# Kernel optimization log

Measured on AMD Instinct MI355X. Metric: run time of the kernel, lower is better.

Reference implementation:

```python
import jax, jax.numpy as jnp
import numpy as np

NUM_HEADS = 8
EPS = 1e-12  # torch F.normalize eps


def _l2norm(t):
    n = jnp.linalg.norm(t, axis=-1, keepdims=True)
    return t / jnp.maximum(n, EPS)


def setup_inputs() -> dict:
    key = jax.random.key(0)
    k1, k2, k3 = jax.random.split(key, 3)
    B, T, N, D = 16, 12, 1024, 128
    x = jax.random.normal(k1, (B, T, N, D), dtype=jnp.float32)
    # Linear(model_dim, 3*model_dim, bias=False): stored as (D, 3D) for x @ W
    W_qkv = jax.random.normal(k2, (D, 3 * D), dtype=jnp.float32) * (1.0 / np.sqrt(D))
    W_out = jax.random.normal(k3, (D, D), dtype=jnp.float32) * (1.0 / np.sqrt(D))
    b_out = jnp.zeros((D,), dtype=jnp.float32)
    return {"x": x, "W_qkv": W_qkv, "W_out": W_out, "b_out": b_out}


def reference(x, W_qkv, W_out, b_out):
    B, T, N, D = x.shape
    H = NUM_HEADS
    hd = D // H
    qkv = x @ W_qkv                                  # (B,T,N,3D)
    q, k, v = jnp.split(qkv, 3, axis=-1)
    # split heads + flatten (B,T) -> b = B*T, matching torch stack/flatten
    qs = _l2norm(q.reshape(B * T, N, H, hd))          # (b,N,H,m)
    ks = _l2norm(k.reshape(B * T, N, H, hd))
    vs = v.reshape(B * T, N, H, hd)
    # linear attention: running kv sum + normalizer
    kvs = jnp.einsum('blhm,blhd->bhmd', ks, vs)       # (b,H,m,d)
    attn_num = jnp.einsum('bnhm,bhmd->bnhd', qs, kvs) + N * vs
    ks_sum = jnp.sum(ks, axis=1)                      # (b,H,m)
    normalizer = jnp.einsum('bnhm,bhm->bnh', qs, ks_sum)[..., None] + N
    out = attn_num / normalizer                       # (b,N,H,d)
    out = out.reshape(B, T, N, D)
    return out @ W_out + b_out
```

## Files before the change

### kernel.cpp

```cpp
#include <hip/hip_runtime.h>
#include <hip/hip_bf16.h>

#define NBATCH 192
#define SEQ    1024
#define DIM    128
#define NH     8
#define EPS    1e-12f

typedef short bf16x8 __attribute__((ext_vector_type(8)));
typedef float f32x4  __attribute__((ext_vector_type(4)));

#define KVSP_F   1572864
#define KSSUM_F  24576
#define WSWT_OFF ((size_t)(KVSP_F + KSSUM_F) * 4)

static __device__ __forceinline__ unsigned short f2bf(float f) {
    unsigned u = __builtin_bit_cast(unsigned, f);
    u += 0x7fff + ((u >> 16) & 1);
    return (unsigned short)(u >> 16);
}

static __device__ __forceinline__ unsigned pk2(float a, float b) {
    __hip_bfloat162 h = __float22bfloat162_rn(make_float2(a, b));
    unsigned r;
    __builtin_memcpy(&r, &h, 4);
    return r;
}
static __device__ __forceinline__ unsigned short bf1(float a) {
    __hip_bfloat16 h = __float2bfloat16(a);
    unsigned short r;
    __builtin_memcpy(&r, &h, 2);
    return r;
}

template <int CTRL>
static __device__ __forceinline__ float dpp_add(float v) {
    int j = __builtin_amdgcn_mov_dpp(__builtin_bit_cast(int, v), CTRL, 0xf, 0xf, false);
    return v + __builtin_bit_cast(float, j);
}
static __device__ __forceinline__ float r16sum(float v) {
    v = dpp_add<0xB1>(v);
    v = dpp_add<0x4E>(v);
    v = dpp_add<0x141>(v);
    v = dpp_add<0x140>(v);
    return v;
}

static __device__ __forceinline__ int strip_addr(int row, int el) {
    return row * 32 + ((((el >> 3) ^ (row & 3)) << 3) | (el & 7));
}

static __device__ __forceinline__ uint2 pack4(float a, float b, float c, float d) {
    uint2 r;
    r.x = pk2(a, b);
    r.y = pk2(c, d);
    return r;
}

static __device__ __forceinline__ bf16x8 cvt8(float4 a, float4 b) {
    uint4 u;
    u.x = pk2(a.x, a.y); u.y = pk2(a.z, a.w);
    u.z = pk2(b.x, b.y); u.w = pk2(b.z, b.w);
    return __builtin_bit_cast(bf16x8, u);
}

static __device__ __forceinline__ bf16x8 gfrag(const unsigned short* __restrict__ wT,
                                               int ct, int ks, int lane) {
    return *reinterpret_cast<const bf16x8*>(wT + ((ct * 4 + ks) * 64 + lane) * 8);
}

__global__ __launch_bounds__(256) void k0_prep(const float* __restrict__ Wqkv,
                                               const float* __restrict__ Wout,
                                               float* __restrict__ kssum_ws,
                                               unsigned short* __restrict__ wsWT) {
    int i = blockIdx.x * 256 + threadIdx.x;
    if (i < KSSUM_F) kssum_ws[i] = 0.0f;
    int which = i >> 14, e = i & 16383;
    int j = e & 7, f = e >> 3;
    int n15 = f & 15, q = (f >> 4) & 3, ks = (f >> 6) & 3, ct = f >> 8;
    int k = ks * 32 + q * 8 + j, n = ct * 16 + n15;
    float v = (which < 3) ? Wqkv[k * 384 + which * 128 + n] : Wout[k * 128 + n];
    wsWT[i] = f2bf(v);
}

__global__ __launch_bounds__(512, 4) void k1_kv(const float* __restrict__ x,
                                                const unsigned short* __restrict__ wsWT,
                                                float* __restrict__ kvs_part,
                                                float* __restrict__ kssum_ws) {
    __shared__ float redf[16384];
    __shared__ unsigned short strips[8192];
    int t = threadIdx.x, w = t >> 6, lane = t & 63, q = lane >> 4, n15 = lane & 15;
    int b = blockIdx.x >> 2, seg = blockIdx.x & 3;
    const unsigned short* wkT = wsWT + 16384;
    const unsigned short* wvT = wsWT + 32768;
    unsigned short* knS = strips + w * 1024;
    unsigned short* vS  = knS + 512;

    bf16x8 ah[2][4];
#pragma unroll
    for (int rs = 0; rs < 2; ++rs) {
        int row = seg * 256 + w * 32 + rs * 16 + n15;
        const float* xr = x + (size_t)(b * SEQ + row) * DIM;
#pragma unroll
        for (int ks = 0; ks < 4; ++ks) {
            float4 p0 = *reinterpret_cast<const float4*>(xr + ks * 32 + q * 8);
            float4 p1 = *reinterpret_cast<const float4*>(xr + ks * 32 + q * 8 + 4);
            ah[rs][ks] = cvt8(p0, p1);
        }
    }

#pragma unroll 1
    for (int ct = 0; ct < 8; ++ct) {
        f32x4 ka[2] = {(f32x4){0,0,0,0}, (f32x4){0,0,0,0}};
        f32x4 va[2] = {(f32x4){0,0,0,0}, (f32x4){0,0,0,0}};
#pragma unroll
        for (int ks = 0; ks < 4; ++ks) {
            bf16x8 kb = gfrag(wkT, ct, ks, lane);
            bf16x8 vb = gfrag(wvT, ct, ks, lane);
#pragma unroll
            for (int rs = 0; rs < 2; ++rs) {
                ka[rs] = __builtin_amdgcn_mfma_f32_16x16x32_bf16(ah[rs][ks], kb, ka[rs], 0, 0, 0);
                va[rs] = __builtin_amdgcn_mfma_f32_16x16x32_bf16(ah[rs][ks], vb, va[rs], 0, 0, 0);
            }
        }
        float ksum = 0.f;
#pragma unroll
        for (int rs = 0; rs < 2; ++rs) {
            float kn[4];
#pragma unroll
            for (int r = 0; r < 4; ++r) {
                float val = ka[rs][r];
                float ssq = r16sum(val * val);
                float di  = 1.0f / fmaxf(sqrtf(ssq), EPS);
                kn[r] = val * di;
                ksum += kn[r];
            }
            *reinterpret_cast<uint2*>(knS + strip_addr(n15, rs * 16 + q * 4)) =
                pack4(kn[0], kn[1], kn[2], kn[3]);
            *reinterpret_cast<uint2*>(vS + strip_addr(n15, rs * 16 + q * 4)) =
                pack4(va[rs][0], va[rs][1], va[rs][2], va[rs][3]);
        }
        bf16x8 aK = *reinterpret_cast<const bf16x8*>(knS + strip_addr(n15, q * 8));
        bf16x8 bV = *reinterpret_cast<const bf16x8*>(vS + strip_addr(n15, q * 8));
        f32x4 kacc = __builtin_amdgcn_mfma_f32_16x16x32_bf16(aK, bV, (f32x4){0,0,0,0}, 0, 0, 0);
#pragma unroll
        for (int r = 0; r < 4; ++r)
            redf[w * 2048 + ct * 256 + (q * 4 + r) * 16 + n15] = kacc[r];
        float s = ksum;
        s += __shfl_xor(s, 16); s += __shfl_xor(s, 32);
        if (lane < 16) atomicAdd(&kssum_ws[b * 128 + ct * 16 + n15], s);
    }

    __syncthreads();
    float* myPart = kvs_part + (size_t)blockIdx.x * 2048;
#pragma unroll
    for (int i = 0; i < 4; ++i) {
        int el = i * 512 + t;
        float s = 0.f;
#pragma unroll
        for (int ww = 0; ww < 8; ++ww) s += redf[ww * 2048 + el];
        myPart[el] = s;
    }
}

__global__ __launch_bounds__(512, 4) void k2_out(const float* __restrict__ x,
                                                 const unsigned short* __restrict__ wsWT,
                                                 const float* __restrict__ kvs_part,
                                                 const float* __restrict__ kssum_ws,
                                                 const float* __restrict__ bout,
                                                 float* __restrict__ out) {
    __shared__ unsigned short lds[24576];
    unsigned short* kvsT   = lds;
    unsigned short* strips = lds + 4096;
    unsigned short* tile   = lds + 8192;
    int t = threadIdx.x, w = t >> 6, lane = t & 63, q = lane >> 4, n15 = lane & 15;
    int b = blockIdx.x >> 2, seg = blockIdx.x & 3, rowbase = seg * 256;
    const unsigned short* wqT = wsWT;
    const unsigned short* wvT = wsWT + 32768;
    const unsigned short* woT = wsWT + 49152;

    {
        int row = t >> 2, part = t & 3, h = row >> 4, d = row & 15;
        const float* kp = kvs_part + (size_t)b * 4 * 2048;
        unsigned es[8];
#pragma unroll
        for (int j = 0; j < 8; j += 2) {
            int m0 = part * 8 + j;
            float lo = 0.f, hi = 0.f;
#pragma unroll
            for (int s = 0; s < 4; ++s) {
                if (m0     < 16) lo += kp[s * 2048 + h * 256 + m0 * 16 + d];
                if (m0 + 1 < 16) hi += kp[s * 2048 + h * 256 + (m0 + 1) * 16 + d];
            }
            es[j] = pk2(lo, hi);
        }
        uint4 v = {es[0], es[2], es[4], es[6]};
        *reinterpret_cast<uint4*>(kvsT + row * 32 + ((part ^ (row & 3)) << 3)) = v;
    }

    unsigned short* myS = strips + w * 512;
    unsigned short* tw  = tile + w * 2048;
    {
        uint2 z = {0, 0};
        *reinterpret_cast<uint2*>(myS + strip_addr(n15, 16 + q * 4)) = z;
    }
    __syncthreads();

    bf16x8 qb[4];
#pragma unroll
    for (int ks = 0; ks < 4; ++ks) qb[ks] = gfrag(wqT, 0, ks, lane);
    float kssh = kssum_ws[b * 128 + n15];

#pragma unroll 1
    for (int rs = 0; rs < 2; ++rs) {
        bf16x8 ahc[4];
        {
            int row = rowbase + w * 32 + rs * 16 + n15;
            const float* xr = x + (size_t)(b * SEQ + row) * DIM;
#pragma unroll
            for (int ks = 0; ks < 4; ++ks) {
                float4 p0 = *reinterpret_cast<const float4*>(xr + ks * 32 + q * 8);
                float4 p1 = *reinterpret_cast<const float4*>(xr + ks * 32 + q * 8 + 4);
                ahc[ks] = cvt8(p0, p1);
            }
        }

#pragma unroll 1
        for (int h = 0; h < 8; ++h) {
            bf16x8 vb0 = gfrag(wvT, h, 0, lane);
            bf16x8 vb1 = gfrag(wvT, h, 1, lane);
            bf16x8 vb2 = gfrag(wvT, h, 2, lane);
            bf16x8 vb3 = gfrag(wvT, h, 3, lane);
            f32x4 qa = (f32x4){0,0,0,0};
            qa = __builtin_amdgcn_mfma_f32_16x16x32_bf16(ahc[0], qb[0], qa, 0, 0, 0);
            qa = __builtin_amdgcn_mfma_f32_16x16x32_bf16(ahc[1], qb[1], qa, 0, 0, 0);
            qa = __builtin_amdgcn_mfma_f32_16x16x32_bf16(ahc[2], qb[2], qa, 0, 0, 0);
            qa = __builtin_amdgcn_mfma_f32_16x16x32_bf16(ahc[3], qb[3], qa, 0, 0, 0);
            f32x4 va = (f32x4){0,0,0,0};
            va = __builtin_amdgcn_mfma_f32_16x16x32_bf16(ahc[0], vb0, va, 0, 0, 0);
            va = __builtin_amdgcn_mfma_f32_16x16x32_bf16(ahc[1], vb1, va, 0, 0, 0);
            va = __builtin_amdgcn_mfma_f32_16x16x32_bf16(ahc[2], vb2, va, 0, 0, 0);
            va = __builtin_amdgcn_mfma_f32_16x16x32_bf16(ahc[3], vb3, va, 0, 0, 0);

            int hn = (h + 1) & 7;
            bf16x8 nqb0 = gfrag(wqT, hn, 0, lane);
            bf16x8 nqb1 = gfrag(wqT, hn, 1, lane);
            bf16x8 nqb2 = gfrag(wqT, hn, 2, lane);
            bf16x8 nqb3 = gfrag(wqT, hn, 3, lane);
            float nkss = kssum_ws[b * 128 + hn * 16 + n15];

            float pv[4];
#pragma unroll
            for (int r = 0; r < 4; ++r) {
                float val = qa[r];
                float ssq = r16sum(val * val);
                float tt  = r16sum(val * kssh);
                float di  = 1.0f / fmaxf(sqrtf(ssq), EPS);
                float inv = 1.0f / (tt * di + (float)SEQ);
                pv[r] = val * di * inv;
                va[r] *= (float)SEQ * inv;
            }
#pragma unroll
            for (int r = 0; r < 4; ++r)
                myS[strip_addr(q * 4 + r, n15)] = bf1(pv[r]);
            bf16x8 aq = *reinterpret_cast<const bf16x8*>(myS + strip_addr(n15, q * 8));
            bf16x8 bk = *reinterpret_cast<const bf16x8*>(kvsT + strip_addr(h * 16 + n15, q * 8));
            va = __builtin_amdgcn_mfma_f32_16x16x32_bf16(aq, bk, va, 0, 0, 0);
#pragma unroll
            for (int r = 0; r < 4; ++r) {
                int rt = q * 4 + r;
                int colg = h * 2 + (n15 >> 3);
                tw[rt * 128 + (((colg ^ rt) << 3) | (n15 & 7))] = bf1(va[r]);
            }
            qb[0] = nqb0; qb[1] = nqb1; qb[2] = nqb2; qb[3] = nqb3;
            kssh = nkss;
        }

        bf16x8 ap[4];
#pragma unroll
        for (int ks = 0; ks < 4; ++ks)
            ap[ks] = *reinterpret_cast<const bf16x8*>(
                tw + n15 * 128 + ((((ks << 2) + q) ^ n15) << 3));
#pragma unroll 1
        for (int ct = 0; ct < 8; ++ct) {
            f32x4 oa = (f32x4){0,0,0,0};
#pragma unroll
            for (int ks = 0; ks < 4; ++ks) {
                bf16x8 bb = gfrag(woT, ct, ks, lane);
                oa = __builtin_amdgcn_mfma_f32_16x16x32_bf16(ap[ks], bb, oa, 0, 0, 0);
            }
            float bo = bout[ct * 16 + n15];
#pragma unroll
            for (int r = 0; r < 4; ++r) {
                int row = rowbase + w * 32 + rs * 16 + q * 4 + r;
                out[(size_t)(b * SEQ + row) * DIM + ct * 16 + n15] = oa[r] + bo;
            }
        }
    }
}

extern "C" void kernel_launch(void* const* d_in, const int* in_sizes, int n_in,
                              void* d_out, int out_size, void* d_ws, size_t ws_size,
                              hipStream_t stream) {
    const float* x    = (const float*)d_in[0];
    const float* Wqkv = (const float*)d_in[1];
    const float* Wout = (const float*)d_in[2];
    const float* bout = (const float*)d_in[3];
    float* out = (float*)d_out;

    float* kvs_part = (float*)d_ws;
    float* kssum_ws = kvs_part + KVSP_F;
    unsigned short* wsWT = (unsigned short*)((char*)d_ws + WSWT_OFF);

    k0_prep<<<dim3(256), dim3(256), 0, stream>>>(Wqkv, Wout, kssum_ws, wsWT);
    k1_kv<<<dim3(768), dim3(512), 0, stream>>>(x, wsWT, kvs_part, kssum_ws);
    k2_out<<<dim3(768), dim3(512), 0, stream>>>(x, wsWT, kvs_part, kssum_ws, bout, out);
}
```

Before: 281.5 us.

## Precompute q·ksum via Wq·ksum projection matrix with one MFMA per row strip

Rather than reducing q·ksum with a 16-lane shuffle reduction for every head, the output kernel precomputes U = Wq_h·ksum_h per batch (a 128x8 matrix) in LDS. It then gets all heads' normalizer dot products with four MFMAs per row strip, picking each head's value by lane shuffle. This removes one r16sum reduction per element and the prefetched-Wq register pipeline, and loads the Q/V weight fragments inline instead. The cost is extra per-block setup reading fp32 Wqkv, more LDS, and an unnormalized-q dot product rounded through bf16, which changes numerics slightly.

Measured after the change: 297.4 us. +5.6%, slower.

```diff
diff --git a/kernel.cpp b/kernel.cpp
--- a/kernel.cpp
+++ b/kernel.cpp
@@ -167,12 +167,14 @@
                                                  const unsigned short* __restrict__ wsWT,
                                                  const float* __restrict__ kvs_part,
                                                  const float* __restrict__ kssum_ws,
+                                                 const float* __restrict__ Wqkv,
                                                  const float* __restrict__ bout,
                                                  float* __restrict__ out) {
-    __shared__ unsigned short lds[24576];
+    __shared__ unsigned short lds[26624];
     unsigned short* kvsT   = lds;
     unsigned short* strips = lds + 4096;
-    unsigned short* tile   = lds + 8192;
+    unsigned short* uLds   = lds + 8192;
+    unsigned short* tile   = lds + 10240;
     int t = threadIdx.x, w = t >> 6, lane = t & 63, q = lane >> 4, n15 = lane & 15;
     int b = blockIdx.x >> 2, seg = blockIdx.x & 3, rowbase = seg * 256;
     const unsigned short* wqT = wsWT;
@@ -198,6 +200,22 @@
         *reinterpret_cast<uint4*>(kvsT + row * 32 + ((part ^ (row & 3)) << 3)) = v;
     }
 
+    {
+#pragma unroll
+        for (int p4 = 0; p4 < 4; ++p4) {
+            int p = t * 4 + p4;
+            int c = p >> 4, h = p & 15;
+            float u = 0.f;
+            if (h < 8) {
+                const float* wr = Wqkv + c * 384 + h * 16;
+                const float* ks = kssum_ws + b * 128 + h * 16;
+#pragma unroll
+                for (int m = 0; m < 16; ++m) u += wr[m] * ks[m];
+            }
+            uLds[(((c >> 5) * 4 + ((c >> 3) & 3)) * 16 + h) * 8 + (c & 7)] = bf1(u);
+        }
+    }
+
     unsigned short* myS = strips + w * 512;
     unsigned short* tw  = tile + w * 2048;
     {
@@ -205,11 +223,6 @@
         *reinterpret_cast<uint2*>(myS + strip_addr(n15, 16 + q * 4)) = z;
     }
     __syncthreads();
-
-    bf16x8 qb[4];
-#pragma unroll
-    for (int ks = 0; ks < 4; ++ks) qb[ks] = gfrag(wqT, 0, ks, lane);
-    float kssh = kssum_ws[b * 128 + n15];
 
 #pragma unroll 1
     for (int rs = 0; rs < 2; ++rs) {
@@ -224,37 +237,31 @@
                 ahc[ks] = cvt8(p0, p1);
             }
         }
+        f32x4 ttC = (f32x4){0,0,0,0};
+#pragma unroll
+        for (int ks = 0; ks < 4; ++ks) {
+            bf16x8 uf = *reinterpret_cast<const bf16x8*>(uLds + (ks * 64 + lane) * 8);
+            ttC = __builtin_amdgcn_mfma_f32_16x16x32_bf16(ahc[ks], uf, ttC, 0, 0, 0);
+        }
 
 #pragma unroll 1
         for (int h = 0; h < 8; ++h) {
-            bf16x8 vb0 = gfrag(wvT, h, 0, lane);
-            bf16x8 vb1 = gfrag(wvT, h, 1, lane);
-            bf16x8 vb2 = gfrag(wvT, h, 2, lane);
-            bf16x8 vb3 = gfrag(wvT, h, 3, lane);
             f32x4 qa = (f32x4){0,0,0,0};
-            qa = __builtin_amdgcn_mfma_f32_16x16x32_bf16(ahc[0], qb[0], qa, 0, 0, 0);
-            qa = __builtin_amdgcn_mfma_f32_16x16x32_bf16(ahc[1], qb[1], qa, 0, 0, 0);
-            qa = __builtin_amdgcn_mfma_f32_16x16x32_bf16(ahc[2], qb[2], qa, 0, 0, 0);
-            qa = __builtin_amdgcn_mfma_f32_16x16x32_bf16(ahc[3], qb[3], qa, 0, 0, 0);
             f32x4 va = (f32x4){0,0,0,0};
-            va = __builtin_amdgcn_mfma_f32_16x16x32_bf16(ahc[0], vb0, va, 0, 0, 0);
-            va = __builtin_amdgcn_mfma_f32_16x16x32_bf16(ahc[1], vb1, va, 0, 0, 0);
-            va = __builtin_amdgcn_mfma_f32_16x16x32_bf16(ahc[2], vb2, va, 0, 0, 0);
-            va = __builtin_amdgcn_mfma_f32_16x16x32_bf16(ahc[3], vb3, va, 0, 0, 0);
-
-            int hn = (h + 1) & 7;
-            bf16x8 nqb0 = gfrag(wqT, hn, 0, lane);
-            bf16x8 nqb1 = gfrag(wqT, hn, 1, lane);
-            bf16x8 nqb2 = gfrag(wqT, hn, 2, lane);
-            bf16x8 nqb3 = gfrag(wqT, hn, 3, lane);
-            float nkss = kssum_ws[b * 128 + hn * 16 + n15];
-
+#pragma unroll
+            for (int ks = 0; ks < 4; ++ks) {
+                bf16x8 qb = gfrag(wqT, h, ks, lane);
+                bf16x8 vb = gfrag(wvT, h, ks, lane);
+                qa = __builtin_amdgcn_mfma_f32_16x16x32_bf16(ahc[ks], qb, qa, 0, 0, 0);
+                va = __builtin_amdgcn_mfma_f32_16x16x32_bf16(ahc[ks], vb, va, 0, 0, 0);
+            }
+            int srcl = (lane & 48) | h;
             float pv[4];
 #pragma unroll
             for (int r = 0; r < 4; ++r) {
                 float val = qa[r];
                 float ssq = r16sum(val * val);
-                float tt  = r16sum(val * kssh);
+                float tt  = __shfl(ttC[r], srcl);
                 float di  = 1.0f / fmaxf(sqrtf(ssq), EPS);
                 float inv = 1.0f / (tt * di + (float)SEQ);
                 pv[r] = val * di * inv;
@@ -272,8 +279,6 @@
                 int colg = h * 2 + (n15 >> 3);
                 tw[rt * 128 + (((colg ^ rt) << 3) | (n15 & 7))] = bf1(va[r]);
             }
-            qb[0] = nqb0; qb[1] = nqb1; qb[2] = nqb2; qb[3] = nqb3;
-            kssh = nkss;
         }
 
         bf16x8 ap[4];
@@ -314,5 +319,5 @@
 
     k0_prep<<<dim3(256), dim3(256), 0, stream>>>(Wqkv, Wout, kssum_ws, wsWT);
     k1_kv<<<dim3(768), dim3(512), 0, stream>>>(x, wsWT, kvs_part, kssum_ws);
-    k2_out<<<dim3(768), dim3(512), 0, stream>>>(x, wsWT, kvs_part, kssum_ws, bout, out);
-}
+    k2_out<<<dim3(768), dim3(512), 0, stream>>>(x, wsWT, kvs_part, kssum_ws, Wqkv, bout, out);
+}
```
